# Performance work log

Measured on AMD Instinct MI355X. Metric: run time of the kernel, lower is better.

The kernel has to match this reference:

```python
import jax, jax.numpy as jnp
import numpy as np

N, C, O, H, S, SHARE = 30000, 128, 128, 8, 16, 8
D = O // H            # mid_planes = 16
OS = O // SHARE       # 16
OFFSETS = [15000, 30000]
EPS = 1e-5


def _knn(p, offsets, k):
    """Exact per-batch KNN (incl. self), chunked to bound memory."""
    n = p.shape[0]
    idx = np.empty((n, k), dtype=np.int64)
    start = 0
    for end in offsets:
        pb = p[start:end]
        sq = (pb * pb).sum(-1)
        for qs in range(0, pb.shape[0], 1024):
            q = pb[qs:qs + 1024]
            d = sq[qs:qs + q.shape[0], None] - 2.0 * (q @ pb.T) + sq[None, :]
            part = np.argpartition(d, k - 1, axis=1)[:, :k]
            idx[start + qs:start + qs + q.shape[0]] = part + start
        start = end
    return idx


def _ln(x, g, b):
    m = x.mean(-1, keepdims=True)
    v = ((x - m) ** 2).mean(-1, keepdims=True)
    return (x - m) / jnp.sqrt(v + EPS) * g + b


def setup_inputs() -> dict:
    rng = np.random.default_rng(0)
    p_np = (rng.standard_normal((N, 3)) * 5.0).astype(np.float32)
    idx = _knn(p_np, OFFSETS, S)

    key = jax.random.key(0)
    ks = jax.random.split(key, 12)

    def lin(k, i, o):
        return (jax.random.normal(k, (i, o), jnp.float32) / np.sqrt(i)).astype(jnp.float32)

    return {
        "p": jnp.asarray(p_np),
        "x": jax.random.normal(ks[0], (N, C), jnp.float32),
        "idx": jnp.asarray(idx),
        "Wq": lin(ks[1], C, O), "bq": jnp.zeros((O,), jnp.float32),
        "Wk": lin(ks[2], C, O), "bk": jnp.zeros((O,), jnp.float32),
        "Wv": lin(ks[3], C, O), "bv": jnp.zeros((O,), jnp.float32),
        "Wp1": lin(ks[4], 3, 3), "bp1": jnp.zeros((3,), jnp.float32),
        "gp": jnp.ones((3,), jnp.float32), "betap": jnp.zeros((3,), jnp.float32),
        "Wp2": lin(ks[5], 3, O), "bp2": jnp.zeros((O,), jnp.float32),
        "gw1": jnp.ones((D,), jnp.float32), "betaw1": jnp.zeros((D,), jnp.float32),
        "Ww1": lin(ks[6], D, OS), "bw1": jnp.zeros((OS,), jnp.float32),
        "gw2": jnp.ones((OS,), jnp.float32), "betaw2": jnp.zeros((OS,), jnp.float32),
        "Ww2": lin(ks[7], OS, OS), "bw2": jnp.zeros((OS,), jnp.float32),
    }


def reference(p, x, idx, Wq, bq, Wk, bk, Wv, bv, Wp1, bp1, gp, betap, Wp2, bp2,
              gw1, betaw1, Ww1, bw1, gw2, betaw2, Ww2, bw2):
    xq = (x @ Wq + bq).reshape(N, H, D)          # (N,H,D)
    xk = x @ Wk + bk                              # (N,O)
    xv = x @ Wv + bv
    kg = xk[idx].reshape(N, S, H, D)              # neighbor gather
    vg = xv[idx].reshape(N, S, H, D)
    pr = p[idx] - p[:, None, :]                   # relative coords (N,S,3)
    pe = jax.nn.relu(_ln(pr @ Wp1 + bp1, gp, betap)) @ Wp2 + bp2  # (N,S,O)
    pe = pe.reshape(N, S, H, D)
    r = kg + pe - xq[:, None]                     # (N,S,H,D)
    w = jax.nn.relu(_ln(r, gw1, betaw1)) @ Ww1 + bw1
    w = jax.nn.relu(_ln(w, gw2, betaw2)) @ Ww2 + bw2  # (N,S,H,OS)
    w = jax.nn.softmax(w.mean(-1), axis=1)        # softmax over the S neighbors
    out = ((vg + pe) * w[..., None]).sum(axis=1)  # weighted neighbor reduce
    return out.reshape(N, O)
```

## Files before the change

kernel.cpp:

```cpp
#include <hip/hip_runtime.h>
#include <math.h>

typedef unsigned int  uint;
typedef unsigned short ushort;

constexpr int NPTS = 30000;
constexpr int NPAD = 30080;
constexpr int CIN  = 128;
constexpr int OC   = 128;
constexpr int NH   = 8;
constexpr int NS   = 16;
constexpr int DH   = 16;
constexpr int OSH  = 16;
constexpr float EPSF = 1e-5f;

typedef __attribute__((ext_vector_type(8))) short  bf16x8;
typedef __attribute__((ext_vector_type(4))) float  f32x4;
typedef __attribute__((ext_vector_type(2))) __fp16 h2;

__device__ __forceinline__ ushort f2bf(float f) {
    uint u = __float_as_uint(f);
    u += 0x7fff + ((u >> 16) & 1);
    return (ushort)(u >> 16);
}
__device__ __forceinline__ ushort f2h(float f) {
    __fp16 h = (__fp16)f;
    return *(ushort*)&h;
}
__device__ __forceinline__ uint pk2(float a, float b) {
    h2 v = __builtin_amdgcn_cvt_pkrtz(a, b);
    return *(uint*)&v;
}
__device__ __forceinline__ h2 asH2(uint u) { return *(h2*)&u; }

#if defined(__has_builtin)
#if __has_builtin(__builtin_elementwise_max)
#define PKMAX(a, b) __builtin_elementwise_max(a, b)
#endif
#endif
#ifndef PKMAX
__device__ __forceinline__ h2 PKMAX(h2 a, h2 b) {
    h2 r; r[0] = a[0] > b[0] ? a[0] : b[0]; r[1] = a[1] > b[1] ? a[1] : b[1]; return r;
}
#endif

constexpr int PK_WW1   = 0;
constexpr int PK_WP2   = 128;
constexpr int PK_BP2   = 320;
constexpr int PK_GW1   = 384;
constexpr int PK_BW1P  = 392;
constexpr int PK_GW2   = 400;
constexpr int PK_BW2P  = 408;
constexpr int PK_RM    = 416;
constexpr int PKF_BW1  = 424;
constexpr int PKF_RMB  = 440;

constexpr int XB_BLOCKS = (NPAD * CIN / 4) / 256;

__global__ __launch_bounds__(256) void prep_kernel(
    const float* __restrict__ x,
    const float* __restrict__ Wq, const float* __restrict__ Wk, const float* __restrict__ Wv,
    const float* __restrict__ Wp2, const float* __restrict__ bp2,
    const float* __restrict__ gw1, const float* __restrict__ betaw1,
    const float* __restrict__ Ww1, const float* __restrict__ bw1,
    const float* __restrict__ gw2, const float* __restrict__ betaw2,
    const float* __restrict__ Ww2, const float* __restrict__ bw2,
    ushort* __restrict__ xb, ushort* __restrict__ WT, uint* __restrict__ PK)
{
    const int b = blockIdx.x;
    const int t = threadIdx.x;
    if (b < XB_BLOCKS) {
        int e   = (b * 256 + t) * 4;
        int row = e >> 7;
        uint2 o = make_uint2(0, 0);
        if (row < NPTS) {
            float4 f = *(const float4*)(x + e);
            o.x = (uint)f2bf(f.x) | ((uint)f2bf(f.y) << 16);
            o.y = (uint)f2bf(f.z) | ((uint)f2bf(f.w) << 16);
        }
        *(uint2*)(xb + e) = o;
    } else if (b < XB_BLOCKS + 3) {
        int mat = b - XB_BLOCKS;
        const float* W = (mat == 0) ? Wq : (mat == 1 ? Wk : Wv);
        ushort* T = WT + mat * OC * CIN;
        if (t < OC) {
            for (int k = 0; k < CIN; ++k)
                T[t * CIN + k] = f2bf(W[k * OC + t]);
        }
    } else {
        float* FPK = (float*)PK;
        if (t < 128) {
            int dp = t >> 4, o = t & 15;
            PK[PK_WW1 + t] = pk2(Ww1[(2 * dp) * OSH + o], Ww1[(2 * dp + 1) * OSH + o]);
        }
        if (t < 192) {
            int c = t >> 6, jj = t & 63;
            PK[PK_WP2 + t] = pk2(Wp2[c * OC + 2 * jj], Wp2[c * OC + 2 * jj + 1]);
        }
        if (t < 64)
            PK[PK_BP2 + t] = pk2(bp2[2 * t], bp2[2 * t + 1]);
        if (t < 8) {
            PK[PK_GW1 + t]  = pk2(gw1[2 * t],    gw1[2 * t + 1]);
            PK[PK_BW1P + t] = pk2(betaw1[2 * t], betaw1[2 * t + 1]);
            PK[PK_GW2 + t]  = pk2(gw2[2 * t],    gw2[2 * t + 1]);
            PK[PK_BW2P + t] = pk2(betaw2[2 * t], betaw2[2 * t + 1]);
            float r0 = 0.f, r1 = 0.f;
            #pragma unroll
            for (int o2 = 0; o2 < OSH; ++o2) {
                r0 += Ww2[(2 * t) * OSH + o2];
                r1 += Ww2[(2 * t + 1) * OSH + o2];
            }
            PK[PK_RM + t] = pk2(r0 * (1.f / OSH), r1 * (1.f / OSH));
        }
        if (t < 16)
            FPK[PKF_BW1 + t] = bw1[t];
        if (t == 16) {
            float acc = 0.f;
            #pragma unroll
            for (int o2 = 0; o2 < OSH; ++o2) acc += bw2[o2];
            FPK[PKF_RMB] = acc * (1.f / OSH);
        }
    }
}

__global__ __launch_bounds__(256) void qkv_mfma(
    const ushort* __restrict__ xb, const ushort* __restrict__ WT,
    const float* __restrict__ bq, const float* __restrict__ bk, const float* __restrict__ bv,
    ushort* __restrict__ yq, ushort* __restrict__ yk, ushort* __restrict__ yv)
{
    const int mat = blockIdx.y;
    const float* bias = (mat == 0) ? bq : (mat == 1 ? bk : bv);
    ushort* y         = (mat == 0) ? yq : (mat == 1 ? yk : yv);
    const ushort* T   = WT + mat * OC * CIN;

    const int n0   = blockIdx.x * 128;
    const int t    = threadIdx.x;
    const int wave = t >> 6;
    const int lane = t & 63;
    const int m16  = lane & 15;
    const int quad = lane >> 4;

    f32x4 acc[2][8];
    #pragma unroll
    for (int mt = 0; mt < 2; ++mt)
        #pragma unroll
        for (int nt = 0; nt < 8; ++nt)
            acc[mt][nt] = (f32x4){0.f, 0.f, 0.f, 0.f};

    const ushort* arow0 = xb + (size_t)(n0 + wave * 32 + m16) * CIN;
    const ushort* arow1 = arow0 + 16 * CIN;

    #pragma unroll
    for (int ks = 0; ks < 4; ++ks) {
        const int kb = ks * 32 + quad * 8;
        bf16x8 a0 = *(const bf16x8*)(arow0 + kb);
        bf16x8 a1 = *(const bf16x8*)(arow1 + kb);
        #pragma unroll
        for (int nt = 0; nt < 8; ++nt) {
            bf16x8 bfr = *(const bf16x8*)(T + (size_t)(nt * 16 + m16) * CIN + kb);
            acc[0][nt] = __builtin_amdgcn_mfma_f32_16x16x32_bf16(a0, bfr, acc[0][nt], 0, 0, 0);
            acc[1][nt] = __builtin_amdgcn_mfma_f32_16x16x32_bf16(a1, bfr, acc[1][nt], 0, 0, 0);
        }
    }

    #pragma unroll
    for (int mt = 0; mt < 2; ++mt) {
        #pragma unroll
        for (int nt = 0; nt < 8; ++nt) {
            const int col = nt * 16 + m16;
            const float bcol = bias[col];
            #pragma unroll
            for (int r = 0; r < 4; ++r) {
                int row = n0 + wave * 32 + mt * 16 + quad * 4 + r;
                if (row < NPTS)
                    y[(size_t)row * OC + col] = f2h(acc[mt][nt][r] + bcol);
            }
        }
    }
}

__global__ __launch_bounds__(128) void attn_kernel(
    const float* __restrict__ p, const int* __restrict__ idx,
    const ushort* __restrict__ xq, const ushort* __restrict__ xk, const ushort* __restrict__ xv,
    const float* __restrict__ Wp1, const float* __restrict__ bp1,
    const float* __restrict__ gp,  const float* __restrict__ betap,
    const uint* __restrict__ PK,
    float* __restrict__ out)
{
    const int n = blockIdx.x;
    const int t = threadIdx.x;
    const int s = t >> 3;
    const int h = t & 7;

    const float* FPK = (const float*)PK;

    __shared__ float s_t[NS][4];
    __shared__ float s_logit[NS][NH];
    __shared__ float s_mx[NH];
    __shared__ float s_inv[NH];
    __shared__ uint  s_c[NS][68];

    if (t < NS) {
        int ss = t;
        int j = idx[n * NS + ss];
        float pr0 = p[j * 3 + 0] - p[n * 3 + 0];
        float pr1 = p[j * 3 + 1] - p[n * 3 + 1];
        float pr2 = p[j * 3 + 2] - p[n * 3 + 2];
        float u[3];
        #pragma unroll
        for (int c = 0; c < 3; ++c)
            u[c] = bp1[c] + pr0 * Wp1[0 * 3 + c] + pr1 * Wp1[1 * 3 + c] + pr2 * Wp1[2 * 3 + c];
        float m   = (u[0] + u[1] + u[2]) * (1.f / 3.f);
        float d0 = u[0] - m, d1 = u[1] - m, d2 = u[2] - m;
        float var = (d0 * d0 + d1 * d1 + d2 * d2) * (1.f / 3.f);
        float inv = rsqrtf(var + EPSF);
        #pragma unroll
        for (int c = 0; c < 3; ++c)
            s_t[ss][c] = fmaxf((u[c] - m) * inv * gp[c] + betap[c], 0.f);
    }
    __syncthreads();

    const int j = idx[n * NS + s];
    const float t0 = s_t[s][0], t1 = s_t[s][1], t2 = s_t[s][2];
    const int obase = h * DH;

    __attribute__((aligned(16))) h2 pe2[8];
    {
        h2 t02 = asH2(pk2(t0, t0));
        h2 t12 = asH2(pk2(t1, t1));
        h2 t22 = asH2(pk2(t2, t2));
        const uint* W0p = PK + PK_WP2 + 0 * 64 + h * 8;
        const uint* W1p = PK + PK_WP2 + 1 * 64 + h * 8;
        const uint* W2p = PK + PK_WP2 + 2 * 64 + h * 8;
        const uint* Bp  = PK + PK_BP2 + h * 8;
        #pragma unroll
        for (int i = 0; i < 8; ++i) {
            h2 acc = asH2(Bp[i]);
            acc = acc + t02 * asH2(W0p[i]);
            acc = acc + t12 * asH2(W1p[i]);
            acc = acc + t22 * asH2(W2p[i]);
            pe2[i] = acc;
        }
    }

    __attribute__((aligned(16))) h2 v2[8], r2[8];
    {
        __attribute__((aligned(16))) h2 k2[8], q2[8];
        const uint4* k4 = (const uint4*)(xk + (size_t)j * OC + obase);
        const uint4* v4 = (const uint4*)(xv + (size_t)j * OC + obase);
        const uint4* q4 = (const uint4*)(xq + (size_t)n * OC + obase);
        *(uint4*)&k2[0] = k4[0]; *(uint4*)&k2[4] = k4[1];
        *(uint4*)&v2[0] = v4[0]; *(uint4*)&v2[4] = v4[1];
        *(uint4*)&q2[0] = q4[0]; *(uint4*)&q2[4] = q4[1];
        #pragma unroll
        for (int i = 0; i < 8; ++i)
            r2[i] = (k2[i] + pe2[i]) - q2[i];
    }

    __attribute__((aligned(16))) h2 a2[8];
    {
        h2 sum2 = r2[0];
        #pragma unroll
        for (int i = 1; i < 8; ++i) sum2 = sum2 + r2[i];
        float m = ((float)sum2[0] + (float)sum2[1]) * (1.f / DH);
        h2 m2 = asH2(pk2(m, m));
        h2 vs2 = {(__fp16)0.f, (__fp16)0.f};
        #pragma unroll
        for (int i = 0; i < 8; ++i) {
            r2[i] = r2[i] - m2;
            vs2 = vs2 + r2[i] * r2[i];
        }
        float var = ((float)vs2[0] + (float)vs2[1]) * (1.f / DH);
        float inv = rsqrtf(var + EPSF);
        h2 inv2 = asH2(pk2(inv, inv));
        h2 z2 = {(__fp16)0.f, (__fp16)0.f};
        #pragma unroll
        for (int i = 0; i < 8; ++i) {
            h2 gi = asH2(PK[PK_GW1 + i]) * inv2;
            a2[i] = PKMAX(r2[i] * gi + asH2(PK[PK_BW1P + i]), z2);
        }
    }

    float w1[OSH];
    #pragma unroll
    for (int o2 = 0; o2 < OSH; ++o2) w1[o2] = FPK[PKF_BW1 + o2];
    #pragma unroll
    for (int dp = 0; dp < 8; ++dp) {
        #pragma unroll
        for (int o2 = 0; o2 < OSH; ++o2)
            w1[o2] = __builtin_amdgcn_fdot2(a2[dp], asH2(PK[PK_WW1 + dp * 16 + o2]), w1[o2], false);
    }

    float logit;
    {
        __attribute__((aligned(16))) h2 w2[8];
        #pragma unroll
        for (int i = 0; i < 8; ++i) w2[i] = asH2(pk2(w1[2 * i], w1[2 * i + 1]));
        h2 sum2 = w2[0];
        #pragma unroll
        for (int i = 1; i < 8; ++i) sum2 = sum2 + w2[i];
        float m = ((float)sum2[0] + (float)sum2[1]) * (1.f / OSH);
        h2 m2 = asH2(pk2(m, m));
        h2 vs2 = {(__fp16)0.f, (__fp16)0.f};
        #pragma unroll
        for (int i = 0; i < 8; ++i) {
            w2[i] = w2[i] - m2;
            vs2 = vs2 + w2[i] * w2[i];
        }
        float var = ((float)vs2[0] + (float)vs2[1]) * (1.f / OSH);
        float inv = rsqrtf(var + EPSF);
        h2 inv2 = asH2(pk2(inv, inv));
        h2 z2 = {(__fp16)0.f, (__fp16)0.f};
        logit = FPK[PKF_RMB];
        #pragma unroll
        for (int i = 0; i < 8; ++i) {
            h2 gi = asH2(PK[PK_GW2 + i]) * inv2;
            h2 bv2 = PKMAX(w2[i] * gi + asH2(PK[PK_BW2P + i]), z2);
            logit = __builtin_amdgcn_fdot2(bv2, asH2(PK[PK_RM + i]), logit, false);
        }
    }

    s_logit[s][h] = logit;
    __syncthreads();

    if (t < NH) {
        float mx = -1e30f;
        #pragma unroll
        for (int ss = 0; ss < NS; ++ss) mx = fmaxf(mx, s_logit[ss][t]);
        float denom = 0.f;
        #pragma unroll
        for (int ss = 0; ss < NS; ++ss) denom += __expf(s_logit[ss][t] - mx);
        s_mx[t] = mx;
        s_inv[t] = 1.f / denom;
    }
    __syncthreads();

    float w = __expf(logit - s_mx[h]) * s_inv[h];

    {
        h2 w2p = asH2(pk2(w, w));
        __attribute__((aligned(16))) h2 c2[8];
        #pragma unroll
        for (int i = 0; i < 8; ++i)
            c2[i] = (v2[i] + pe2[i]) * w2p;
        *(uint4*)&s_c[s][h * 8]     = *(uint4*)&c2[0];
        *(uint4*)&s_c[s][h * 8 + 4] = *(uint4*)&c2[4];
    }
    __syncthreads();

    {
        const int oh = t >> 4;
        const int od = t & 15;
        const int col = oh * 8 + (od >> 1);
        h2 acc2 = {(__fp16)0.f, (__fp16)0.f};
        #pragma unroll
        for (int ss = 0; ss < NS; ++ss)
            acc2 = acc2 + asH2(s_c[ss][col]);
        out[(size_t)n * OC + t] = (float)acc2[od & 1];
    }
}

extern "C" void kernel_launch(void* const* d_in, const int* in_sizes, int n_in,
                              void* d_out, int out_size, void* d_ws, size_t ws_size,
                              hipStream_t stream) {
    const float* p     = (const float*)d_in[0];
    const float* x     = (const float*)d_in[1];
    const int*   idx   = (const int*)d_in[2];
    const float* Wq    = (const float*)d_in[3];
    const float* bq    = (const float*)d_in[4];
    const float* Wk    = (const float*)d_in[5];
    const float* bk    = (const float*)d_in[6];
    const float* Wv    = (const float*)d_in[7];
    const float* bv    = (const float*)d_in[8];
    const float* Wp1   = (const float*)d_in[9];
    const float* bp1   = (const float*)d_in[10];
    const float* gp    = (const float*)d_in[11];
    const float* betap = (const float*)d_in[12];
    const float* Wp2   = (const float*)d_in[13];
    const float* bp2   = (const float*)d_in[14];
    const float* gw1   = (const float*)d_in[15];
    const float* betaw1= (const float*)d_in[16];
    const float* Ww1   = (const float*)d_in[17];
    const float* bw1   = (const float*)d_in[18];
    const float* gw2   = (const float*)d_in[19];
    const float* betaw2= (const float*)d_in[20];
    const float* Ww2   = (const float*)d_in[21];
    const float* bw2   = (const float*)d_in[22];
    float* out = (float*)d_out;

    ushort* xb = (ushort*)d_ws;
    ushort* WT = xb + (size_t)NPAD * CIN;
    ushort* xq = WT + 3 * OC * CIN;
    ushort* xk = xq + (size_t)NPTS * OC;
    ushort* xv = xk + (size_t)NPTS * OC;
    uint*   PACKS = (uint*)(xv + (size_t)NPTS * OC);

    prep_kernel<<<XB_BLOCKS + 4, 256, 0, stream>>>(x, Wq, Wk, Wv,
                                                   Wp2, bp2, gw1, betaw1,
                                                   Ww1, bw1, gw2, betaw2, Ww2, bw2,
                                                   xb, WT, PACKS);

    dim3 g1(NPAD / 128, 3);
    qkv_mfma<<<g1, 256, 0, stream>>>(xb, WT, bq, bk, bv, xq, xk, xv);

    attn_kernel<<<NPTS, 128, 0, stream>>>(p, idx, xq, xk, xv,
                                          Wp1, bp1, gp, betap,
                                          PACKS, out);
}
```

Baseline: 196.2 us.

## Remap threads so softmax uses warp shuffles; compute pos-encoding per thread

```diff
diff --git a/kernel.cpp b/kernel.cpp
--- a/kernel.cpp
+++ b/kernel.cpp
@@ -189,20 +189,17 @@
 {
     const int n = blockIdx.x;
     const int t = threadIdx.x;
-    const int s = t >> 3;
-    const int h = t & 7;
+    const int s = t & 15;
+    const int h = t >> 4;
 
     const float* FPK = (const float*)PK;
 
-    __shared__ float s_t[NS][4];
-    __shared__ float s_logit[NS][NH];
-    __shared__ float s_mx[NH];
-    __shared__ float s_inv[NH];
-    __shared__ uint  s_c[NS][68];
-
-    if (t < NS) {
-        int ss = t;
-        int j = idx[n * NS + ss];
+    __shared__ uint s_c[NS][68];
+
+    const int j = idx[n * NS + s];
+
+    float t0, t1, t2;
+    {
         float pr0 = p[j * 3 + 0] - p[n * 3 + 0];
         float pr1 = p[j * 3 + 1] - p[n * 3 + 1];
         float pr2 = p[j * 3 + 2] - p[n * 3 + 2];
@@ -214,14 +211,11 @@
         float d0 = u[0] - m, d1 = u[1] - m, d2 = u[2] - m;
         float var = (d0 * d0 + d1 * d1 + d2 * d2) * (1.f / 3.f);
         float inv = rsqrtf(var + EPSF);
-        #pragma unroll
-        for (int c = 0; c < 3; ++c)
-            s_t[ss][c] = fmaxf((u[c] - m) * inv * gp[c] + betap[c], 0.f);
-    }
-    __syncthreads();
-
-    const int j = idx[n * NS + s];
-    const float t0 = s_t[s][0], t1 = s_t[s][1], t2 = s_t[s][2];
+        t0 = fmaxf((u[0] - m) * inv * gp[0] + betap[0], 0.f);
+        t1 = fmaxf((u[1] - m) * inv * gp[1] + betap[1], 0.f);
+        t2 = fmaxf((u[2] - m) * inv * gp[2] + betap[2], 0.f);
+    }
+
     const int obase = h * DH;
 
     __attribute__((aligned(16))) h2 pe2[8];
@@ -320,22 +314,19 @@
         }
     }
 
-    s_logit[s][h] = logit;
-    __syncthreads();
-
-    if (t < NH) {
-        float mx = -1e30f;
-        #pragma unroll
-        for (int ss = 0; ss < NS; ++ss) mx = fmaxf(mx, s_logit[ss][t]);
-        float denom = 0.f;
-        #pragma unroll
-        for (int ss = 0; ss < NS; ++ss) denom += __expf(s_logit[ss][t] - mx);
-        s_mx[t] = mx;
-        s_inv[t] = 1.f / denom;
-    }
-    __syncthreads();
-
-    float w = __expf(logit - s_mx[h]) * s_inv[h];
+    float w;
+    {
+        float mx = logit;
+        #pragma unroll
+        for (int mask = 1; mask < 16; mask <<= 1)
+            mx = fmaxf(mx, __shfl_xor(mx, mask));
+        float e = __expf(logit - mx);
+        float den = e;
+        #pragma unroll
+        for (int mask = 1; mask < 16; mask <<= 1)
+            den += __shfl_xor(den, mask);
+        w = e / den;
+    }
 
     {
         h2 w2p = asH2(pk2(w, w));
```

Result: no change. 196.0 us (-0.1%).
